# Performance work log

Hardware: AMD Instinct MI355X
Metric: run time of the kernel (lower is better)

## Reference

```python
import jax, jax.numpy as jnp
from jax import lax
import numpy as np

BOHR = 0.52917721067  # Angstrom per Bohr (au.BOHR)
DAMP_MUTUAL = 0.39
DAMP_FIELD = 0.7
N_ITER = 7  # fixed-point iterations for induced dipoles


def setup_inputs() -> dict:
    key = jax.random.key(0)
    N = 100000
    deg = 32
    E = N * deg
    k1, k2, k3, k4, k5, k6, k7 = jax.random.split(key, 7)
    edge_src = jax.random.randint(k1, (E,), 0, N)
    edge_dst = jax.random.randint(k2, (E,), 0, N)
    # realistic interatomic distances in [1, 6] Angstrom (avoid r ~ 0)
    distances = 1.0 + 5.0 * jax.random.uniform(k3, (E,), dtype=jnp.float32)
    u = jax.random.normal(k4, (E, 3), dtype=jnp.float32)
    u = u / jnp.linalg.norm(u, axis=-1, keepdims=True)
    vec = u * distances[:, None]  # consistent |vec| == distances
    polarisability = 0.5 + 1.5 * jax.random.uniform(k5, (N,), dtype=jnp.float32)
    charges = 0.3 * jax.random.normal(k6, (N,), dtype=jnp.float32)
    species = jax.random.randint(k7, (N,), 1, 10)
    return {
        "species": species,
        "edge_src": edge_src,
        "edge_dst": edge_dst,
        "distances": distances,
        "vec": vec,
        "polarisability": polarisability,
        "charges": charges,
    }


def reference(species, edge_src, edge_dst, distances, vec, polarisability, charges):
    N = polarisability.shape[0]
    # convert to atomic units
    rij = distances / BOHR                      # [E]
    vec_ij = vec / BOHR                         # [E,3]
    pol = polarisability.reshape(-1) / BOHR**3  # [N]

    # Thole damping: u_ij^3 = r^3 / sqrt(alpha_i * alpha_j)
    alpha_ij = pol[edge_src] * pol[edge_dst]
    uij3 = rij**3 / jnp.sqrt(alpha_ij)
    exp_m = jnp.exp(-DAMP_MUTUAL * uij3)
    l3_m = 1.0 - exp_m
    l5_m = 1.0 - (1.0 + DAMP_MUTUAL * uij3) * exp_m
    l3_f = 1.0 - jnp.exp(-DAMP_FIELD * uij3)

    inv_r3 = 1.0 / rij**3
    inv_r5 = inv_r3 / rij**2

    # permanent (charge) electric field at src atoms, Thole-damped
    e_edges = (l3_f * charges[edge_dst] * inv_r3)[:, None] * vec_ij  # [E,3]
    E0 = jax.ops.segment_sum(e_edges, edge_src, num_segments=N)      # [N,3]

    alpha = pol[:, None]  # isotropic polarisability [N,1]

    def matvec(mu):
        # Thole-damped dipole-dipole interaction tensor applied to mu: (T mu)_i
        mu_d = mu[edge_dst]                                   # [E,3]
        dot = jnp.sum(vec_ij * mu_d, axis=-1)                 # [E]
        t = (l3_m * inv_r3)[:, None] * mu_d \
            - (3.0 * l5_m * inv_r5 * dot)[:, None] * vec_ij   # [E,3]
        return jax.ops.segment_sum(t, edge_src, num_segments=N)

    # iterative induced dipoles: mu = alpha * (E0 - T mu)
    mu0 = alpha * E0

    def step(mu, _):
        return alpha * (E0 - matvec(mu)), None

    mu, _ = lax.scan(step, mu0, None, length=N_ITER)

    # per-atom polarisation energy: -1/2 mu . E0
    energy = -0.5 * jnp.sum(mu * E0, axis=-1)  # [N]
    return energy
```

## Files before the change

### kernel.cpp

```cpp
#include <hip/hip_runtime.h>
#include <hip/hip_fp16.h>


static constexpr float INV_B  = 1.0f / 0.52917721067f;
static constexpr float INV_B3 = INV_B * INV_B * INV_B;
static constexpr float DM = 0.39f;
static constexpr float DF = 0.7f;
static constexpr int   NITER = 7;
#define SCAN_B 512
#define CHUNK 8192
#define MAXBUCK 512

__device__ inline unsigned packh2(float a, float b) {
    return (unsigned)__half_as_ushort(__float2half_rn(a)) |
           ((unsigned)__half_as_ushort(__float2half_rn(b)) << 16);
}
__device__ inline float unph_lo(unsigned u) {
    return __half2float(__ushort_as_half((unsigned short)(u & 0xFFFFu)));
}
__device__ inline float unph_hi(unsigned u) {
    return __half2float(__ushort_as_half((unsigned short)(u >> 16)));
}


__global__ void bhist_kernel(const int* __restrict__ esrc, int* __restrict__ hraw,
                             int* __restrict__ hpad, int E, int nbuck, int nblk)
{
    __shared__ int cnt[MAXBUCK];
    int tid = threadIdx.x, blk = blockIdx.x;
    for (int b = tid; b < nbuck; b += blockDim.x) cnt[b] = 0;
    __syncthreads();
    int lo = blk * CHUNK, hi = min(E, lo + CHUNK);
    for (int i = lo + tid; i < hi; i += blockDim.x)
        atomicAdd(&cnt[esrc[i] >> 8], 1);
    __syncthreads();
    for (int b = tid; b < nbuck; b += blockDim.x) {
        int c = cnt[b];
        hraw[b * nblk + blk] = c;
        hpad[b * nblk + blk] = (c + 3) & ~3;
    }
}


__global__ void scan1_kernel(const int* __restrict__ in, int* __restrict__ excl,
                             int* __restrict__ blocksum, int n)
{
    __shared__ int sh[SCAN_B];
    int tid = threadIdx.x;
    int i = blockIdx.x * SCAN_B + tid;
    int v = (i < n) ? in[i] : 0;
    sh[tid] = v;
    __syncthreads();
    for (int off = 1; off < SCAN_B; off <<= 1) {
        int t = (tid >= off) ? sh[tid - off] : 0;
        __syncthreads();
        sh[tid] += t;
        __syncthreads();
    }
    if (i < n) excl[i] = sh[tid] - v;
    if (tid == SCAN_B - 1) blocksum[blockIdx.x] = sh[tid];
}

__global__ void scan2_kernel(int* __restrict__ blocksum, int nb)
{
    __shared__ int sh[512];
    int tid = threadIdx.x;
    int v = (tid < nb) ? blocksum[tid] : 0;
    sh[tid] = v;
    __syncthreads();
    for (int off = 1; off < 512; off <<= 1) {
        int t = (tid >= off) ? sh[tid - off] : 0;
        __syncthreads();
        sh[tid] += t;
        __syncthreads();
    }
    if (tid < nb) blocksum[tid] = sh[tid] - v;
}

__global__ void scan3_kernel(int* __restrict__ excl, const int* __restrict__ blocksum, int n)
{
    int i = blockIdx.x * SCAN_B + threadIdx.x;
    if (i < n) excl[i] += blocksum[blockIdx.x];
}

__global__ void bktptr_kernel(const int* __restrict__ hoffpad, const int* __restrict__ hpad,
                              int* __restrict__ bktptr, int nbuck, int nblk, int nScan)
{
    int b = blockIdx.x * blockDim.x + threadIdx.x;
    if (b < nbuck) bktptr[b] = hoffpad[b * nblk];
    if (b == nbuck) bktptr[b] = hoffpad[nScan - 1] + hpad[nScan - 1];
}


__global__ void build_kernel(const int* __restrict__ esrc, const int* __restrict__ edst,
                             const float* __restrict__ dist, const float* __restrict__ vec,
                             const float* __restrict__ pol, const float* __restrict__ chg,
                             const int* __restrict__ hoffpad, const int* __restrict__ hpad,
                             uint4* __restrict__ recs, int E, int nbuck, int nblk)
{
    __shared__ int cur[MAXBUCK];
    int tid = threadIdx.x, blk = blockIdx.x;
    for (int b = tid; b < nbuck; b += blockDim.x) cur[b] = hoffpad[b * nblk + blk];
    __syncthreads();
    int lo = blk * CHUNK, hi = min(E, lo + CHUNK);
    for (int i = lo + tid; i < hi; i += blockDim.x) {
        int s = esrc[i], d = edst[i];
        float r  = dist[i] * INV_B;
        float vx = vec[3*i+0] * INV_B;
        float vy = vec[3*i+1] * INV_B;
        float vz = vec[3*i+2] * INV_B;
        float ps = pol[s] * INV_B3;
        float pd = pol[d] * INV_B3;
        float r2 = r * r;
        float r3 = r2 * r;
        float u  = r3 * rsqrtf(ps * pd);
        float em = __expf(-DM * u);
        float l3m = 1.0f - em;
        float l5m = 1.0f - (1.0f + DM * u) * em;
        float inv_r3 = 1.0f / r3;
        float inv_r5 = inv_r3 / r2;
        float c1 = l3m * inv_r3;
        float sw = sqrtf(3.0f * l5m * inv_r5);
        float ec = (1.0f - __expf(-DF * u)) * chg[d] * inv_r3;
        float g  = ec / sw;
        int slot = atomicAdd(&cur[s >> 8], 1);
        uint4 rc;
        rc.x = (unsigned)(d | ((s & 255) << 20));
        rc.y = __float_as_uint(c1);
        rc.z = packh2(sw * vx, sw * vy);
        rc.w = packh2(sw * vz, g);
        recs[slot] = rc;
    }
    __syncthreads();
    for (int b = tid; b < nbuck; b += blockDim.x) {
        int base = hoffpad[b * nblk + blk];
        int end  = base + hpad[b * nblk + blk];
        for (int s = cur[b]; s < end; ++s) recs[s] = make_uint4(0, 0, 0, 0);
    }
}


__global__ void sort_kernel(const int* __restrict__ bktptr, const int* __restrict__ hoffraw,
                            int nblk, const uint4* __restrict__ recs_raw,
                            uint4* __restrict__ recs_srt,
                            int* __restrict__ rowbeg, int* __restrict__ rowend, int N)
{
    __shared__ int hist[256];
    __shared__ int scn[256];
    __shared__ int cur[256];
    int tid = threadIdx.x, b = blockIdx.x;
    int j0 = bktptr[b], j1 = bktptr[b + 1];
    int tight0 = hoffraw[b * nblk];
    hist[tid] = 0;
    __syncthreads();
    for (int j = j0 + tid; j < j1; j += 256) {
        uint4 rc = recs_raw[j];
        if (rc.y) atomicAdd(&hist[rc.x >> 20], 1);
    }
    __syncthreads();
    int cnt = hist[tid];
    scn[tid] = cnt;
    __syncthreads();
    for (int off = 1; off < 256; off <<= 1) {
        int t = (tid >= off) ? scn[tid - off] : 0;
        __syncthreads();
        scn[tid] += t;
        __syncthreads();
    }
    int beg = tight0 + scn[tid] - cnt;
    cur[tid] = beg;
    int row = b * 256 + tid;
    if (row < N) { rowbeg[row] = beg; rowend[row] = beg + cnt; }
    __syncthreads();
    for (int j = j0 + tid; j < j1; j += 256) {
        uint4 rc = recs_raw[j];
        if (rc.y) {
            int slot = atomicAdd(&cur[rc.x >> 20], 1);
            recs_srt[slot] = rc;
        }
    }
}


__global__ void e0g_kernel(const int* __restrict__ rowbeg, const int* __restrict__ rowend,
                           const uint4* __restrict__ recs, const float* __restrict__ pol,
                           float4* __restrict__ E0, float4* __restrict__ mu, int N)
{
    int tid  = threadIdx.x;
    int lane = tid & 15;
    int row  = (blockIdx.x * blockDim.x + tid) >> 4;
    if (row >= N) return;
    int r0 = rowbeg[row], r1 = rowend[row];
    float sx = 0.f, sy = 0.f, sz = 0.f;
    for (int j = r0 + lane; j < r1; j += 16) {
        uint4 rc = recs[j];
        float g = unph_hi(rc.w);
        sx += g * unph_lo(rc.z);
        sy += g * unph_hi(rc.z);
        sz += g * unph_lo(rc.w);
    }
    for (int m = 8; m >= 1; m >>= 1) {
        sx += __shfl_xor(sx, m);
        sy += __shfl_xor(sy, m);
        sz += __shfl_xor(sz, m);
    }
    if (lane == 0) {
        E0[row] = make_float4(sx, sy, sz, 0.f);
        float a = pol[row] * INV_B3;
        mu[row] = make_float4(a * sx, a * sy, a * sz, 0.f);
    }
}

__global__ void mvg_kernel(const int* __restrict__ rowbeg, const int* __restrict__ rowend,
                           const uint4* __restrict__ recs, const float4* __restrict__ E0,
                           const float* __restrict__ pol,
                           const float4* __restrict__ mu_in, float4* __restrict__ mu_out,
                           float* __restrict__ energy, int N, int final_iter)
{
    int tid  = threadIdx.x;
    int lane = tid & 15;
    int row  = (blockIdx.x * blockDim.x + tid) >> 4;
    if (row >= N) return;
    int r0 = rowbeg[row], r1 = rowend[row];
    float ax = 0.f, ay = 0.f, az = 0.f;
    for (int j = r0 + lane; j < r1; j += 16) {
        uint4 rc = recs[j];
        float4 m = mu_in[rc.x & 0xFFFFF];
        float c1 = __uint_as_float(rc.y);
        float wx = unph_lo(rc.z), wy = unph_hi(rc.z), wz = unph_lo(rc.w);
        float dot = wx * m.x + wy * m.y + wz * m.z;
        ax += c1 * m.x - dot * wx;
        ay += c1 * m.y - dot * wy;
        az += c1 * m.z - dot * wz;
    }
    for (int msk = 8; msk >= 1; msk >>= 1) {
        ax += __shfl_xor(ax, msk);
        ay += __shfl_xor(ay, msk);
        az += __shfl_xor(az, msk);
    }
    if (lane == 0) {
        float4 e0 = E0[row];
        float a = pol[row] * INV_B3;
        float mx = a * (e0.x - ax);
        float my = a * (e0.y - ay);
        float mz = a * (e0.z - az);
        mu_out[row] = make_float4(mx, my, mz, 0.f);
        if (final_iter)
            energy[row] = -0.5f * (mx * e0.x + my * e0.y + mz * e0.z);
    }
}


__global__ void e0b_kernel(const int* __restrict__ bktptr, const uint4* __restrict__ recs,
                           const float* __restrict__ pol,
                           float4* __restrict__ E0, float4* __restrict__ mu, int N)
{
    __shared__ float acc[256 * 3];
    int tid = threadIdx.x, b = blockIdx.x;
    for (int k = tid; k < 768; k += 256) acc[k] = 0.f;
    __syncthreads();
    int j0 = bktptr[b], j1 = bktptr[b + 1];
    for (int j = j0 + tid; j < j1; j += 256) {
        uint4 rc = recs[j];
        int lr = (int)(rc.x >> 20) & 255;
        float g = unph_hi(rc.w);
        atomicAdd(&acc[lr*3+0], g * unph_lo(rc.z));
        atomicAdd(&acc[lr*3+1], g * unph_hi(rc.z));
        atomicAdd(&acc[lr*3+2], g * unph_lo(rc.w));
    }
    __syncthreads();
    int r = b * 256 + tid;
    if (r < N) {
        float ax = acc[tid*3], ay = acc[tid*3+1], az = acc[tid*3+2];
        E0[r] = make_float4(ax, ay, az, 0.f);
        float a = pol[r] * INV_B3;
        mu[r] = make_float4(a * ax, a * ay, a * az, 0.f);
    }
}

__global__ void mvb_kernel(const int* __restrict__ bktptr, const uint4* __restrict__ recs,
                           const float4* __restrict__ E0, const float* __restrict__ pol,
                           const float4* __restrict__ mu_in, float4* __restrict__ mu_out,
                           float* __restrict__ energy, int N, int final_iter)
{
    __shared__ float acc[256 * 3];
    int tid = threadIdx.x, b = blockIdx.x;
    for (int k = tid; k < 768; k += 256) acc[k] = 0.f;
    __syncthreads();
    int j0 = bktptr[b], j1 = bktptr[b + 1];
    for (int j = j0 + tid; j < j1; j += 256) {
        uint4 rc = recs[j];
        float4 m = mu_in[rc.x & 0xFFFFF];
        float c1 = __uint_as_float(rc.y);
        float wx = unph_lo(rc.z), wy = unph_hi(rc.z), wz = unph_lo(rc.w);
        float dot = wx * m.x + wy * m.y + wz * m.z;
        int lr = (int)(rc.x >> 20) & 255;
        atomicAdd(&acc[lr*3+0], c1 * m.x - dot * wx);
        atomicAdd(&acc[lr*3+1], c1 * m.y - dot * wy);
        atomicAdd(&acc[lr*3+2], c1 * m.z - dot * wz);
    }
    __syncthreads();
    int r = b * 256 + tid;
    if (r < N) {
        float4 e0 = E0[r];
        float a = pol[r] * INV_B3;
        float mx = a * (e0.x - acc[tid*3+0]);
        float my = a * (e0.y - acc[tid*3+1]);
        float mz = a * (e0.z - acc[tid*3+2]);
        mu_out[r] = make_float4(mx, my, mz, 0.f);
        if (final_iter)
            energy[r] = -0.5f * (mx * e0.x + my * e0.y + mz * e0.z);
    }
}


__global__ void fb_e0_kernel(const int* esrc, const int* edst, const float* dist,
                             const float* vec, const float* pol, const float* chg,
                             float4* E0, int E)
{
    int e = blockIdx.x * blockDim.x + threadIdx.x;
    if (e >= E) return;
    int s = esrc[e], d = edst[e];
    float r  = dist[e] * INV_B;
    float vx = vec[3*e+0]*INV_B, vy = vec[3*e+1]*INV_B, vz = vec[3*e+2]*INV_B;
    float r3 = r*r*r;
    float u  = r3 * rsqrtf(pol[s]*INV_B3 * pol[d]*INV_B3);
    float ec = (1.0f - __expf(-DF*u)) * chg[d] / r3;
    atomicAdd(&E0[s].x, ec*vx); atomicAdd(&E0[s].y, ec*vy); atomicAdd(&E0[s].z, ec*vz);
}

__global__ void fb_init_kernel(const float* pol, const float4* E0, float4* mu, float4* acc, int N)
{
    int i = blockIdx.x * blockDim.x + threadIdx.x;
    if (i >= N) return;
    float a = pol[i]*INV_B3; float4 e0 = E0[i];
    mu[i]  = make_float4(a*e0.x, a*e0.y, a*e0.z, 0.f);
    acc[i] = make_float4(0.f,0.f,0.f,0.f);
}

__global__ void fb_matvec_kernel(const int* esrc, const int* edst, const float* dist,
                                 const float* vec, const float* pol,
                                 const float4* mu, float4* acc, int E)
{
    int e = blockIdx.x * blockDim.x + threadIdx.x;
    if (e >= E) return;
    int s = esrc[e], d = edst[e];
    float r  = dist[e]*INV_B;
    float vx = vec[3*e+0]*INV_B, vy = vec[3*e+1]*INV_B, vz = vec[3*e+2]*INV_B;
    float r2 = r*r, r3 = r2*r;
    float u  = r3 * rsqrtf(pol[s]*INV_B3 * pol[d]*INV_B3);
    float em = __expf(-DM*u);
    float c1 = (1.0f - em) / r3;
    float c2 = 3.0f * (1.0f - (1.0f + DM*u)*em) / (r3*r2);
    float4 m = mu[d];
    float k = c2 * (vx*m.x + vy*m.y + vz*m.z);
    atomicAdd(&acc[s].x, c1*m.x - k*vx);
    atomicAdd(&acc[s].y, c1*m.y - k*vy);
    atomicAdd(&acc[s].z, c1*m.z - k*vz);
}

__global__ void fb_update_kernel(const float* pol, const float4* E0, float4* acc,
                                 float4* mu, float* energy, int N, int final_iter)
{
    int i = blockIdx.x * blockDim.x + threadIdx.x;
    if (i >= N) return;
    float a = pol[i]*INV_B3; float4 e0 = E0[i]; float4 ac = acc[i];
    float mx = a*(e0.x-ac.x), my = a*(e0.y-ac.y), mz = a*(e0.z-ac.z);
    mu[i]  = make_float4(mx,my,mz,0.f);
    acc[i] = make_float4(0.f,0.f,0.f,0.f);
    if (final_iter) energy[i] = -0.5f*(mx*e0.x + my*e0.y + mz*e0.z);
}


static inline size_t align_up(size_t x, size_t a) { return (x + a - 1) & ~(a - 1); }

extern "C" void kernel_launch(void* const* d_in, const int* in_sizes, int n_in,
                              void* d_out, int out_size, void* d_ws, size_t ws_size,
                              hipStream_t stream)
{
    const int*   esrc = (const int*)  d_in[1];
    const int*   edst = (const int*)  d_in[2];
    const float* dist = (const float*)d_in[3];
    const float* vec  = (const float*)d_in[4];
    const float* pol  = (const float*)d_in[5];
    const float* chg  = (const float*)d_in[6];
    const int E = in_sizes[1];
    const int N = in_sizes[5];
    float* out = (float*)d_out;

    const int nbuck = (N + 255) >> 8;
    const int nblk  = (E + CHUNK - 1) / CHUNK;
    const int nScan = nbuck * nblk;
    const int g1    = (nScan + SCAN_B - 1) / SCAN_B;
    const size_t Epad = (size_t)E + 3u * (size_t)nScan;

    char* ws = (char*)d_ws;
    size_t off = 0;
    auto carve = [&](size_t bytes) { size_t o = off; off = align_up(off + bytes, 256); return o; };
    size_t o_hpad    = carve((size_t)nScan * 4);
    size_t o_hoffpad = carve((size_t)nScan * 4);
    size_t o_bsum1   = carve(512 * 4);
    size_t o_bkt     = carve((size_t)(nbuck + 1) * 4);
    size_t o_E0      = carve((size_t)N * 16);
    size_t o_mua     = carve((size_t)N * 16);
    size_t o_mub     = carve((size_t)N * 16);
    size_t o_hraw    = carve((size_t)nScan * 4);
    size_t o_recsraw = carve(Epad * 16);
    size_t need_mid  = off;
    size_t o_hoffraw = carve((size_t)nScan * 4);
    size_t o_bsum2   = carve(512 * 4);
    size_t o_rowbeg  = carve((size_t)N * 4);
    size_t o_rowend  = carve((size_t)N * 4);
    size_t o_recssrt = carve((size_t)E * 16);
    size_t need_sort = off;

    bool shape_ok = (nbuck <= MAXBUCK) && (g1 <= 512) && (nbuck >= 1) && (N < (1 << 20));
    bool ok_sort = shape_ok && (ws_size >= need_sort);
    bool ok_mid  = shape_ok && (ws_size >= need_mid);

    if (ok_sort || ok_mid) {
        int*    hpad    = (int*)   (ws + o_hpad);
        int*    hoffpad = (int*)   (ws + o_hoffpad);
        int*    bsum1   = (int*)   (ws + o_bsum1);
        int*    bktptr  = (int*)   (ws + o_bkt);
        float4* E0      = (float4*)(ws + o_E0);
        float4* mu_a    = (float4*)(ws + o_mua);
        float4* mu_b    = (float4*)(ws + o_mub);
        int*    hraw    = (int*)   (ws + o_hraw);
        uint4*  recsraw = (uint4*) (ws + o_recsraw);

        bhist_kernel<<<nblk, 256, 0, stream>>>(esrc, hraw, hpad, E, nbuck, nblk);
        scan1_kernel<<<g1, SCAN_B, 0, stream>>>(hpad, hoffpad, bsum1, nScan);
        scan2_kernel<<<1, 512, 0, stream>>>(bsum1, g1);
        scan3_kernel<<<g1, SCAN_B, 0, stream>>>(hoffpad, bsum1, nScan);
        bktptr_kernel<<<(nbuck + 256) / 256, 256, 0, stream>>>(hoffpad, hpad, bktptr,
                                                               nbuck, nblk, nScan);
        build_kernel<<<nblk, 256, 0, stream>>>(esrc, edst, dist, vec, pol, chg,
                                               hoffpad, hpad, recsraw, E, nbuck, nblk);

        if (ok_sort) {
            int*   hoffraw = (int*)  (ws + o_hoffraw);
            int*   bsum2   = (int*)  (ws + o_bsum2);
            int*   rowbeg  = (int*)  (ws + o_rowbeg);
            int*   rowend  = (int*)  (ws + o_rowend);
            uint4* recssrt = (uint4*)(ws + o_recssrt);

            scan1_kernel<<<g1, SCAN_B, 0, stream>>>(hraw, hoffraw, bsum2, nScan);
            scan2_kernel<<<1, 512, 0, stream>>>(bsum2, g1);
            scan3_kernel<<<g1, SCAN_B, 0, stream>>>(hoffraw, bsum2, nScan);
            sort_kernel<<<nbuck, 256, 0, stream>>>(bktptr, hoffraw, nblk,
                                                   recsraw, recssrt, rowbeg, rowend, N);

            const int NG16 = (N + 15) / 16;
            e0g_kernel<<<NG16, 256, 0, stream>>>(rowbeg, rowend, recssrt, pol, E0, mu_a, N);
            float4* min_ = mu_a; float4* mout_ = mu_b;
            for (int it = 0; it < NITER; ++it) {
                mvg_kernel<<<NG16, 256, 0, stream>>>(rowbeg, rowend, recssrt, E0, pol,
                                                     min_, mout_, out, N, it == NITER - 1);
                float4* t = min_; min_ = mout_; mout_ = t;
            }
        } else {
            e0b_kernel<<<nbuck, 256, 0, stream>>>(bktptr, recsraw, pol, E0, mu_a, N);
            float4* min_ = mu_a; float4* mout_ = mu_b;
            for (int it = 0; it < NITER; ++it) {
                mvb_kernel<<<nbuck, 256, 0, stream>>>(bktptr, recsraw, E0, pol,
                                                      min_, mout_, out, N, it == NITER - 1);
                float4* t = min_; min_ = mout_; mout_ = t;
            }
        }
    } else {
        float4* E0  = (float4*)(ws);
        float4* mu  = (float4*)(ws + (size_t)N * 16);
        float4* acc = (float4*)(ws + (size_t)N * 32);
        const int EB = 256, NB = 256;
        const int EG = (E + EB - 1) / EB;
        const int NG = (N + NB - 1) / NB;
        hipMemsetAsync(E0, 0, (size_t)N * 16, stream);
        fb_e0_kernel<<<EG, EB, 0, stream>>>(esrc, edst, dist, vec, pol, chg, E0, E);
        fb_init_kernel<<<NG, NB, 0, stream>>>(pol, E0, mu, acc, N);
        for (int it = 0; it < NITER; ++it) {
            fb_matvec_kernel<<<EG, EB, 0, stream>>>(esrc, edst, dist, vec, pol, mu, acc, E);
            fb_update_kernel<<<NG, NB, 0, stream>>>(pol, E0, acc, mu, out, N, it == NITER - 1);
        }
    }
}
```

Baseline: 337.0 us.

## Split sorted edge records into 12-byte matvec stream plus separate field array

The sort kernel now writes a 12-byte per-edge record (dst index, half-packed c1 and direction components) plus a separate float array holding the permanent-field coefficient. The matvec loop, which runs seven times, reads 12 instead of 16 bytes per edge. Build and histogram kernels get larger chunks and 1024 threads, and the sort kernel uses 512 threads with per-bucket padding raised to 8. Storing c1 as fp16 lowers its precision, and the strided 12-byte loads may coalesce less well than aligned 16-byte loads.

```diff
diff --git a/kernel.cpp b/kernel.cpp
--- a/kernel.cpp
+++ b/kernel.cpp
@@ -8,7 +8,8 @@
 static constexpr float DF = 0.7f;
 static constexpr int   NITER = 7;
 #define SCAN_B 512
-#define CHUNK 8192
+#define CHUNK 16384
+#define BUILD_T 1024
 #define MAXBUCK 512
 
 __device__ inline unsigned packh2(float a, float b) {
@@ -37,7 +38,7 @@
     for (int b = tid; b < nbuck; b += blockDim.x) {
         int c = cnt[b];
         hraw[b * nblk + blk] = c;
-        hpad[b * nblk + blk] = (c + 3) & ~3;
+        hpad[b * nblk + blk] = (c + 7) & ~7;
     }
 }
 
@@ -142,7 +143,7 @@
 
 __global__ void sort_kernel(const int* __restrict__ bktptr, const int* __restrict__ hoffraw,
                             int nblk, const uint4* __restrict__ recs_raw,
-                            uint4* __restrict__ recs_srt,
+                            unsigned* __restrict__ srt, float* __restrict__ gsrt,
                             int* __restrict__ rowbeg, int* __restrict__ rowend, int N)
 {
     __shared__ int hist[256];
@@ -151,39 +152,49 @@
     int tid = threadIdx.x, b = blockIdx.x;
     int j0 = bktptr[b], j1 = bktptr[b + 1];
     int tight0 = hoffraw[b * nblk];
-    hist[tid] = 0;
-    __syncthreads();
-    for (int j = j0 + tid; j < j1; j += 256) {
+    if (tid < 256) hist[tid] = 0;
+    __syncthreads();
+    for (int j = j0 + tid; j < j1; j += blockDim.x) {
         uint4 rc = recs_raw[j];
         if (rc.y) atomicAdd(&hist[rc.x >> 20], 1);
     }
     __syncthreads();
-    int cnt = hist[tid];
-    scn[tid] = cnt;
+    if (tid < 256) scn[tid] = hist[tid];
     __syncthreads();
     for (int off = 1; off < 256; off <<= 1) {
-        int t = (tid >= off) ? scn[tid - off] : 0;
+        int t = 0;
+        if (tid < 256 && tid >= off) t = scn[tid - off];
         __syncthreads();
-        scn[tid] += t;
+        if (tid < 256) scn[tid] += t;
         __syncthreads();
     }
-    int beg = tight0 + scn[tid] - cnt;
-    cur[tid] = beg;
-    int row = b * 256 + tid;
-    if (row < N) { rowbeg[row] = beg; rowend[row] = beg + cnt; }
-    __syncthreads();
-    for (int j = j0 + tid; j < j1; j += 256) {
+    if (tid < 256) {
+        int cnt = hist[tid];
+        int beg = tight0 + scn[tid] - cnt;
+        cur[tid] = beg;
+        int row = b * 256 + tid;
+        if (row < N) { rowbeg[row] = beg; rowend[row] = beg + cnt; }
+    }
+    __syncthreads();
+    for (int j = j0 + tid; j < j1; j += blockDim.x) {
         uint4 rc = recs_raw[j];
         if (rc.y) {
             int slot = atomicAdd(&cur[rc.x >> 20], 1);
-            recs_srt[slot] = rc;
+            float c1 = __uint_as_float(rc.y);
+            float wx = unph_lo(rc.z);
+            srt[3*slot+0] = rc.x;
+            srt[3*slot+1] = packh2(c1, wx);
+            srt[3*slot+2] = rc.w;
+            srt[3*slot+2] = packh2(unph_hi(rc.z), unph_lo(rc.w));
+            gsrt[slot] = unph_hi(rc.w);
         }
     }
 }
 
 
 __global__ void e0g_kernel(const int* __restrict__ rowbeg, const int* __restrict__ rowend,
-                           const uint4* __restrict__ recs, const float* __restrict__ pol,
+                           const unsigned* __restrict__ srt, const float* __restrict__ gsrt,
+                           const float* __restrict__ pol,
                            float4* __restrict__ E0, float4* __restrict__ mu, int N)
 {
     int tid  = threadIdx.x;
@@ -193,11 +204,12 @@
     int r0 = rowbeg[row], r1 = rowend[row];
     float sx = 0.f, sy = 0.f, sz = 0.f;
     for (int j = r0 + lane; j < r1; j += 16) {
-        uint4 rc = recs[j];
-        float g = unph_hi(rc.w);
-        sx += g * unph_lo(rc.z);
-        sy += g * unph_hi(rc.z);
-        sz += g * unph_lo(rc.w);
+        unsigned w0 = srt[3*j+1];
+        unsigned w1 = srt[3*j+2];
+        float g = gsrt[j];
+        sx += g * unph_hi(w0);
+        sy += g * unph_lo(w1);
+        sz += g * unph_hi(w1);
     }
     for (int m = 8; m >= 1; m >>= 1) {
         sx += __shfl_xor(sx, m);
@@ -212,7 +224,7 @@
 }
 
 __global__ void mvg_kernel(const int* __restrict__ rowbeg, const int* __restrict__ rowend,
-                           const uint4* __restrict__ recs, const float4* __restrict__ E0,
+                           const unsigned* __restrict__ srt, const float4* __restrict__ E0,
                            const float* __restrict__ pol,
                            const float4* __restrict__ mu_in, float4* __restrict__ mu_out,
                            float* __restrict__ energy, int N, int final_iter)
@@ -224,10 +236,12 @@
     int r0 = rowbeg[row], r1 = rowend[row];
     float ax = 0.f, ay = 0.f, az = 0.f;
     for (int j = r0 + lane; j < r1; j += 16) {
-        uint4 rc = recs[j];
-        float4 m = mu_in[rc.x & 0xFFFFF];
-        float c1 = __uint_as_float(rc.y);
-        float wx = unph_lo(rc.z), wy = unph_hi(rc.z), wz = unph_lo(rc.w);
+        unsigned pk = srt[3*j+0];
+        unsigned w0 = srt[3*j+1];
+        unsigned w1 = srt[3*j+2];
+        float4 m = mu_in[pk & 0xFFFFF];
+        float c1 = unph_lo(w0);
+        float wx = unph_hi(w0), wy = unph_lo(w1), wz = unph_hi(w1);
         float dot = wx * m.x + wy * m.y + wz * m.z;
         ax += c1 * m.x - dot * wx;
         ay += c1 * m.y - dot * wy;
@@ -392,7 +406,7 @@
     const int nblk  = (E + CHUNK - 1) / CHUNK;
     const int nScan = nbuck * nblk;
     const int g1    = (nScan + SCAN_B - 1) / SCAN_B;
-    const size_t Epad = (size_t)E + 3u * (size_t)nScan;
+    const size_t Epad = (size_t)E + 7u * (size_t)nScan;
 
     char* ws = (char*)d_ws;
     size_t off = 0;
@@ -411,7 +425,8 @@
     size_t o_bsum2   = carve(512 * 4);
     size_t o_rowbeg  = carve((size_t)N * 4);
     size_t o_rowend  = carve((size_t)N * 4);
-    size_t o_recssrt = carve((size_t)E * 16);
+    size_t o_srt     = carve((size_t)E * 12);
+    size_t o_gsrt    = carve((size_t)E * 4);
     size_t need_sort = off;
 
     bool shape_ok = (nbuck <= MAXBUCK) && (g1 <= 512) && (nbuck >= 1) && (N < (1 << 20));
@@ -429,33 +444,34 @@
         int*    hraw    = (int*)   (ws + o_hraw);
         uint4*  recsraw = (uint4*) (ws + o_recsraw);
 
-        bhist_kernel<<<nblk, 256, 0, stream>>>(esrc, hraw, hpad, E, nbuck, nblk);
+        bhist_kernel<<<nblk, BUILD_T, 0, stream>>>(esrc, hraw, hpad, E, nbuck, nblk);
         scan1_kernel<<<g1, SCAN_B, 0, stream>>>(hpad, hoffpad, bsum1, nScan);
         scan2_kernel<<<1, 512, 0, stream>>>(bsum1, g1);
         scan3_kernel<<<g1, SCAN_B, 0, stream>>>(hoffpad, bsum1, nScan);
         bktptr_kernel<<<(nbuck + 256) / 256, 256, 0, stream>>>(hoffpad, hpad, bktptr,
                                                                nbuck, nblk, nScan);
-        build_kernel<<<nblk, 256, 0, stream>>>(esrc, edst, dist, vec, pol, chg,
-                                               hoffpad, hpad, recsraw, E, nbuck, nblk);
+        build_kernel<<<nblk, BUILD_T, 0, stream>>>(esrc, edst, dist, vec, pol, chg,
+                                                   hoffpad, hpad, recsraw, E, nbuck, nblk);
 
         if (ok_sort) {
-            int*   hoffraw = (int*)  (ws + o_hoffraw);
-            int*   bsum2   = (int*)  (ws + o_bsum2);
-            int*   rowbeg  = (int*)  (ws + o_rowbeg);
-            int*   rowend  = (int*)  (ws + o_rowend);
-            uint4* recssrt = (uint4*)(ws + o_recssrt);
+            int*      hoffraw = (int*)     (ws + o_hoffraw);
+            int*      bsum2   = (int*)     (ws + o_bsum2);
+            int*      rowbeg  = (int*)     (ws + o_rowbeg);
+            int*      rowend  = (int*)     (ws + o_rowend);
+            unsigned* srt     = (unsigned*)(ws + o_srt);
+            float*    gsrt    = (float*)   (ws + o_gsrt);
 
             scan1_kernel<<<g1, SCAN_B, 0, stream>>>(hraw, hoffraw, bsum2, nScan);
             scan2_kernel<<<1, 512, 0, stream>>>(bsum2, g1);
             scan3_kernel<<<g1, SCAN_B, 0, stream>>>(hoffraw, bsum2, nScan);
-            sort_kernel<<<nbuck, 256, 0, stream>>>(bktptr, hoffraw, nblk,
-                                                   recsraw, recssrt, rowbeg, rowend, N);
+            sort_kernel<<<nbuck, 512, 0, stream>>>(bktptr, hoffraw, nblk, recsraw,
+                                                   srt, gsrt, rowbeg, rowend, N);
 
             const int NG16 = (N + 15) / 16;
-            e0g_kernel<<<NG16, 256, 0, stream>>>(rowbeg, rowend, recssrt, pol, E0, mu_a, N);
+            e0g_kernel<<<NG16, 256, 0, stream>>>(rowbeg, rowend, srt, gsrt, pol, E0, mu_a, N);
             float4* min_ = mu_a; float4* mout_ = mu_b;
             for (int it = 0; it < NITER; ++it) {
-                mvg_kernel<<<NG16, 256, 0, stream>>>(rowbeg, rowend, recssrt, E0, pol,
+                mvg_kernel<<<NG16, 256, 0, stream>>>(rowbeg, rowend, srt, E0, pol,
                                                      min_, mout_, out, N, it == NITER - 1);
                 float4* t = min_; min_ = mout_; mout_ = t;
             }
```

After: 336.6 us. About the same (-0.1%).
